# Kernel tuning notes

Hardware: AMD Instinct MI355X
Metric: run time of the kernel (lower is better)

## Reference

```python
import jax, jax.numpy as jnp
import numpy as np

LATENT, HIDDEN, NF, MAXN = 256, 512, 64, 50
B = 128
# ordered node pairs (i, j), i != j, in the original double-loop (row-major) order
_pairs = np.array([(i, j) for i in range(MAXN) for j in range(MAXN) if i != j], dtype=np.int32)
II = jnp.asarray(_pairs[:, 0])  # [P]
JJ = jnp.asarray(_pairs[:, 1])  # [P]


def _lin_init(key, out_d, in_d):
    kw, kb = jax.random.split(key)
    s = 1.0 / np.sqrt(in_d)
    W = jax.random.uniform(kw, (out_d, in_d), jnp.float32, -s, s)
    b = jax.random.uniform(kb, (out_d,), jnp.float32, -s, s)
    return W, b


def setup_inputs() -> dict:
    key = jax.random.key(0)
    ks = jax.random.split(key, 7)
    z = jax.random.normal(ks[0], (B, LATENT), jnp.float32)
    # node decoder: latent -> hidden -> hidden -> maxn*nf
    W1, b1 = _lin_init(ks[1], HIDDEN, LATENT)
    W2, b2 = _lin_init(ks[2], HIDDEN, HIDDEN)
    W3, b3 = _lin_init(ks[3], MAXN * NF, HIDDEN)
    # edge decoder: latent + 2*nf -> hidden -> hidden//2 -> 1
    E1, c1 = _lin_init(ks[4], HIDDEN, LATENT + 2 * NF)
    E2, c2 = _lin_init(ks[5], HIDDEN // 2, HIDDEN)
    E3, c3 = _lin_init(ks[6], 1, HIDDEN // 2)
    return {"z": z, "W1": W1, "b1": b1, "W2": W2, "b2": b2, "W3": W3, "b3": b3,
            "E1": E1, "c1": c1, "E2": E2, "c2": c2, "E3": E3, "c3": c3}


def reference(z, W1, b1, W2, b2, W3, b3, E1, c1, E2, c2, E3, c3):
    # ---- node decoder ----
    h = jax.nn.relu(z @ W1.T + b1)
    h = jax.nn.relu(h @ W2.T + b2)
    node_feat = (h @ W3.T + b3).reshape(B, MAXN, NF)  # raw logits used for edges
    node_probs = jax.nn.sigmoid(node_feat)
    # ---- edge decoder: batched over all P = MAXN*(MAXN-1) ordered pairs ----
    ni = node_feat[:, II, :]  # [B, P, NF]
    nj = node_feat[:, JJ, :]  # [B, P, NF]
    P = II.shape[0]
    zb = jnp.broadcast_to(z[:, None, :], (B, P, LATENT))
    edge_in = jnp.concatenate([zb, ni, nj], axis=-1)  # [B, P, LATENT+2*NF]
    e = jax.nn.relu(jnp.einsum("bpf,hf->bph", edge_in, E1) + c1)
    e = jax.nn.relu(jnp.einsum("bph,gh->bpg", e, E2) + c2)
    edge_probs = jax.nn.sigmoid(jnp.einsum("bpg,og->bpo", e, E3) + c3)[..., 0]  # [B, P]
    return node_probs, edge_probs
```

## Files before the change

kernel.cpp:

```cpp
#include <hip/hip_runtime.h>
#include <hip/hip_bf16.h>
#include <math.h>

#define LATENT 256
#define HIDDEN 512
#define NFD    64
#define MAXN   50
#define BATCH  128
#define NPAIR  2450
#define PTILE  64
#define NTILES 39

typedef __attribute__((ext_vector_type(8))) _Float16 f16x8;
typedef __attribute__((ext_vector_type(4))) float f32x4;
typedef __attribute__((ext_vector_type(4))) unsigned int u32x4;

__device__ __forceinline__ float sigmoidf_(float x) {
    return 1.0f / (1.0f + expf(-x));
}
__device__ __forceinline__ f16x8 build_e1(f16x8 ui, f16x8 uj) {
    f16x8 s = ui + uj;
    return __builtin_elementwise_max(s, (f16x8)(_Float16)0);
}
__device__ __forceinline__ u32x4 pack8(float4 a, float4 b) {
    f16x8 h;
    h[0] = (_Float16)a.x; h[1] = (_Float16)a.y;
    h[2] = (_Float16)a.z; h[3] = (_Float16)a.w;
    h[4] = (_Float16)b.x; h[5] = (_Float16)b.y;
    h[6] = (_Float16)b.z; h[7] = (_Float16)b.w;
    return __builtin_bit_cast(u32x4, h);
}

__global__ __launch_bounds__(256) void prologue_a(
    const float* __restrict__ z,
    const float* __restrict__ W1, const float* __restrict__ b1,
    const float* __restrict__ E1, const float* __restrict__ c1,
    const float* __restrict__ E2, const float* __restrict__ W2,
    const float* __restrict__ W3,
    unsigned short* __restrict__ E2t,
    unsigned short* __restrict__ W2t,
    unsigned short* __restrict__ W3t,
    unsigned short* __restrict__ E1ih,
    unsigned short* __restrict__ E1jh,
    unsigned short* __restrict__ h1h, float* __restrict__ Abc)
{
    const int tid = threadIdx.x;

    if (blockIdx.x >= 32) {
        int slot = (blockIdx.x - 32) * 4 + blockIdx.y;
        int e = (slot * 256 + tid) * 8;
        float4 a, b;
        unsigned short* dst;
        if (e < 262144) {
            int row = e >> 9, k = e & 511;
            a = *(const float4*)&W2[e];
            b = *(const float4*)&W2[e + 4];
            dst = W2t + (((k >> 3) * 512 + row) << 3);
        } else if (e < 1900544) {
            int l = e - 262144;
            int grow = l >> 9, k = l & 511;
            int node = grow >> 6, row = grow & 63;
            a = *(const float4*)&W3[l];
            b = *(const float4*)&W3[l + 4];
            dst = W3t + node * 32768 + (((k >> 3) * 64 + row) << 3);
        } else if (e < 1933312) {
            int l = e - 1900544; int row = l >> 6, col = l & 63;
            a = *(const float4*)&E1[row * 384 + 256 + col];
            b = *(const float4*)&E1[row * 384 + 260 + col];
            dst = E1ih + l;
        } else {
            int l = e - 1933312; int row = l >> 6, col = l & 63;
            a = *(const float4*)&E1[row * 384 + 320 + col];
            b = *(const float4*)&E1[row * 384 + 324 + col];
            dst = E1jh + l;
        }
        *(u32x4*)dst = pack8(a, b);
        return;
    }

    if (blockIdx.x >= 16) {
        int idx = ((blockIdx.x - 16) * 4 + blockIdx.y) * 256 + tid;
        int g  = idx & 255;
        int kc = idx >> 8;
        float4 a = *(const float4*)&E2[(size_t)g * 512 + kc * 8];
        float4 b = *(const float4*)&E2[(size_t)g * 512 + kc * 8 + 4];
        *(u32x4*)(E2t + (size_t)idx * 8) = pack8(a, b);
        return;
    }

    __shared__ __align__(16) float As[16][34];
    __shared__ __align__(16) float Bs[16][68];

    const int m0 = blockIdx.y * 32;
    const int n0 = blockIdx.x * 64;
    const bool isE = n0 >= 512;
    const float* Bp = isE ? E1 + (size_t)(n0 - 512) * 384 : W1 + (size_t)n0 * 256;
    const int ldb = isE ? 384 : 256;

    const int sra = tid >> 3;
    const int kca = (tid & 7) * 2;
    const int srb = tid >> 2;
    const int kcb = (tid & 3) * 4;
    const int tx = tid & 15;
    const int ty = tid >> 4;

    float acc[2][4] = {};

    for (int k0 = 0; k0 < 256; k0 += 16) {
        float2 a2 = *(const float2*)&z[(size_t)(m0 + sra) * 256 + k0 + kca];
        As[kca][sra] = a2.x; As[kca + 1][sra] = a2.y;
        float4 b4 = *(const float4*)&Bp[(size_t)srb * ldb + k0 + kcb];
        Bs[kcb + 0][srb] = b4.x; Bs[kcb + 1][srb] = b4.y;
        Bs[kcb + 2][srb] = b4.z; Bs[kcb + 3][srb] = b4.w;
        __syncthreads();
        #pragma unroll
        for (int k = 0; k < 16; ++k) {
            float av[2], bv[4];
            av[0] = As[k][ty * 2]; av[1] = As[k][ty * 2 + 1];
            *(float4*)bv = *(const float4*)&Bs[k][tx * 4];
            #pragma unroll
            for (int r = 0; r < 2; ++r)
                #pragma unroll
                for (int c = 0; c < 4; ++c)
                    acc[r][c] = fmaf(av[r], bv[c], acc[r][c]);
        }
        __syncthreads();
    }

    #pragma unroll
    for (int r = 0; r < 2; ++r) {
        int gm = m0 + ty * 2 + r;
        #pragma unroll
        for (int c = 0; c < 4; ++c) {
            int gn = n0 + tx * 4 + c;
            if (isE) {
                int gl = gn - 512;
                Abc[(size_t)gm * 512 + gl] = acc[r][c] + c1[gl];
            } else {
                float v = fmaxf(acc[r][c] + b1[gn], 0.f);
                h1h[(size_t)gm * 512 + gn] =
                    __builtin_bit_cast(unsigned short, (_Float16)v);
            }
        }
    }
}

__global__ __launch_bounds__(512, 1) void nfu_gemm(
    const unsigned short* __restrict__ h1h,
    const unsigned short* __restrict__ W2t,
    const float* __restrict__ b2,
    const unsigned short* __restrict__ W3t,
    const float* __restrict__ b3,
    const unsigned short* __restrict__ E1ih,
    const unsigned short* __restrict__ E1jh,
    const float* __restrict__ Abc,
    float* __restrict__ outN,
    unsigned short* __restrict__ Uih,
    unsigned short* __restrict__ Ujh)
{
    __shared__ unsigned short As[2][64 * 32];
    __shared__ __align__(16) unsigned short h2s[64][520];
    __shared__ __align__(16) unsigned short nft[64][72];

    const int tid = threadIdx.x;
    const int lane = tid & 63;
    const int w8 = tid >> 6;
    const int w  = w8 & 3;
    const int ln = lane & 15;
    const int hi = lane >> 4;
    const int node = blockIdx.x;
    const int m0 = blockIdx.y * 64;

    const int srow = (tid & 255) >> 2;
    const int sc   = tid & 3;
    const unsigned short* gA = h1h + (size_t)(m0 + srow) * 512 + sc * 8;
    const int swr = srow * 32 + ((sc ^ ((srow >> 1) & 3)) * 8);
    const int q   = hi ^ ((ln >> 1) & 3);
    const int ard = ln * 32 + q * 8;
    const unsigned short* bB = W2t + ((size_t)hi * 512 + 64 * w8 + ln) * 8;

    f32x4 acc[4][4] = {};
    f16x8 hN = {};
    if (tid < 256) {
        f16x8 h0 = *(const f16x8*)gA;
        *(f16x8*)&As[0][swr] = h0;
        hN = *(const f16x8*)(gA + 32);
    }
    f16x8 bf[4];
    #pragma unroll
    for (int ni = 0; ni < 4; ++ni)
        bf[ni] = *(const f16x8*)(bB + ni * 128);
    asm volatile("s_waitcnt lgkmcnt(0)\n\ts_barrier" ::: "memory");

    #pragma unroll
    for (int ks = 0; ks < 16; ++ks) {
        if (tid < 256 && ks < 15)
            *(f16x8*)&As[(ks + 1) & 1][swr] = hN;
        if (tid < 256 && ks < 14)
            hN = *(const f16x8*)(gA + 32 * (ks + 2));
        f16x8 af[4];
        #pragma unroll
        for (int mi = 0; mi < 4; ++mi)
            af[mi] = *(const f16x8*)&As[ks & 1][ard + mi * 512];
        __builtin_amdgcn_s_setprio(1);
        #pragma unroll
        for (int ni = 0; ni < 4; ++ni)
            #pragma unroll
            for (int mi = 0; mi < 4; ++mi)
                acc[mi][ni] = __builtin_amdgcn_mfma_f32_16x16x32_f16(
                    af[mi], bf[ni], acc[mi][ni], 0, 0, 0);
        __builtin_amdgcn_s_setprio(0);
        if (ks < 15) {
            #pragma unroll
            for (int ni = 0; ni < 4; ++ni)
                bf[ni] = *(const f16x8*)(bB + (size_t)(ks + 1) * 16384 + ni * 128);
            asm volatile("s_waitcnt lgkmcnt(0)\n\ts_barrier" ::: "memory");
        }
    }

    #pragma unroll
    for (int ni = 0; ni < 4; ++ni) {
        int col = 64 * w8 + 16 * ni + ln;
        float bias = b2[col];
        #pragma unroll
        for (int mi = 0; mi < 4; ++mi)
            #pragma unroll
            for (int r = 0; r < 4; ++r) {
                float v = fmaxf(acc[mi][ni][r] + bias, 0.f);
                h2s[16 * mi + 4 * hi + r][col] =
                    __builtin_bit_cast(unsigned short, (_Float16)v);
            }
    }
    __syncthreads();

    if (w8 < 4) {
        const unsigned short* bW3 = W3t + (size_t)node * 32768 + hi * 512 + ln * 8;
        f32x4 accB[4] = {};
        #pragma unroll
        for (int ks = 0; ks < 16; ++ks) {
            f16x8 af = *(const f16x8*)&h2s[16 * w + ln][ks * 32 + hi * 8];
            f16x8 bfB[4];
            #pragma unroll
            for (int ni = 0; ni < 4; ++ni)
                bfB[ni] = *(const f16x8*)(bW3 + ks * 2048 + ni * 128);
            #pragma unroll
            for (int ni = 0; ni < 4; ++ni)
                accB[ni] = __builtin_amdgcn_mfma_f32_16x16x32_f16(
                    af, bfB[ni], accB[ni], 0, 0, 0);
        }
        #pragma unroll
        for (int ni = 0; ni < 4; ++ni) {
            int gnl = 16 * ni + ln;
            int gng = node * 64 + gnl;
            float bias = b3[gng];
            #pragma unroll
            for (int r = 0; r < 4; ++r) {
                int bl = 16 * w + 4 * hi + r;
                float v = accB[ni][r] + bias;
                outN[(size_t)(m0 + bl) * 3200 + gng] = sigmoidf_(v);
                nft[bl][gnl] = __builtin_bit_cast(unsigned short, (_Float16)v);
            }
        }
    }
    __syncthreads();

    if (w8 < 4) {
        f16x8 af2[2][4];
        #pragma unroll
        for (int ks2 = 0; ks2 < 2; ++ks2)
            #pragma unroll
            for (int mi = 0; mi < 4; ++mi)
                af2[ks2][mi] = *(const f16x8*)&nft[16 * mi + ln][ks2 * 32 + hi * 8];

        #pragma unroll
        for (int ij = 0; ij < 2; ++ij) {
            const unsigned short* Ep = ij ? E1jh : E1ih;
            unsigned short* Ud = ij ? Ujh : Uih;
            #pragma unroll
            for (int half = 0; half < 2; ++half) {
                f32x4 acc2[4][4] = {};
                #pragma unroll
                for (int ks2 = 0; ks2 < 2; ++ks2) {
                    f16x8 bf2[4];
                    #pragma unroll
                    for (int ni = 0; ni < 4; ++ni)
                        bf2[ni] = *(const f16x8*)(Ep +
                            (size_t)(128 * w + half * 64 + 16 * ni + ln) * 64 +
                            ks2 * 32 + hi * 8);
                    #pragma unroll
                    for (int ni = 0; ni < 4; ++ni)
                        #pragma unroll
                        for (int mi = 0; mi < 4; ++mi)
                            acc2[mi][ni] = __builtin_amdgcn_mfma_f32_16x16x32_f16(
                                af2[ks2][mi], bf2[ni], acc2[mi][ni], 0, 0, 0);
                }
                #pragma unroll
                for (int mi = 0; mi < 4; ++mi) {
                    #pragma unroll
                    for (int r = 0; r < 4; ++r) {
                        int batch = m0 + 16 * mi + 4 * hi + r;
                        #pragma unroll
                        for (int ni = 0; ni < 4; ++ni) {
                            int h = 128 * w + half * 64 + 16 * ni + ln;
                            float v = acc2[mi][ni][r];
                            if (ij == 0) v += Abc[(size_t)batch * 512 + h];
                            Ud[((size_t)batch * 50 + node) * 512 + h] =
                                __builtin_bit_cast(unsigned short, (_Float16)v);
                        }
                    }
                }
            }
        }
    }
}

__global__ __launch_bounds__(256, 4) void edge_mfma(
    const unsigned short* __restrict__ Ui,
    const unsigned short* __restrict__ Uj,
    const unsigned short* __restrict__ E2t,
    const float* __restrict__ c2,
    const float* __restrict__ E3,
    const float* __restrict__ c3p,
    float* __restrict__ outE)
{
    __shared__ unsigned short As[2][PTILE * 32];
    __shared__ float c2_s[256], e3_s[256];
    __shared__ int   ii_s[PTILE], jj_s[PTILE];
    __shared__ float red[PTILE][5];

    const int gid = blockIdx.x;
    const int nid = (gid & 7) * 624 + (gid >> 3);
    const int b   = nid / NTILES;
    const int p0  = (nid - b * NTILES) * PTILE;

    const int tid = threadIdx.x;
    const int lane = tid & 63;
    const int wid  = tid >> 6;
    const int ln = lane & 15;
    const int hi = lane >> 4;

    c2_s[tid] = c2[tid];
    e3_s[tid] = E3[tid];
    if (tid < PTILE) {
        int p = p0 + tid;
        int i = 0, j = 0;
        if (p < NPAIR) {
            i = p / 49;
            int kk = p - i * 49;
            j = kk + (kk >= i ? 1 : 0);
        }
        ii_s[tid] = i;
        jj_s[tid] = j;
    }
    __syncthreads();

    const unsigned short* UiB = Ui + (size_t)b * MAXN * HIDDEN;
    const unsigned short* UjB = Uj + (size_t)b * MAXN * HIDDEN;

    const int srow = tid >> 2;
    const int sc   = tid & 3;
    const unsigned short* gUi = UiB + (size_t)ii_s[srow] * HIDDEN + sc * 8;
    const unsigned short* gUj = UjB + (size_t)jj_s[srow] * HIDDEN + sc * 8;
    const int swr = srow * 32 + ((sc ^ ((srow >> 1) & 3)) * 8);

    const int q   = hi ^ ((ln >> 1) & 3);
    const int ard = ln * 32 + q * 8;

    const unsigned short* bB = E2t + ((size_t)hi * 256 + 64 * wid + ln) * 8;

    f32x4 acc[4][4] = {};

    {
        f16x8 u0 = *(const f16x8*)gUi;
        f16x8 v0 = *(const f16x8*)gUj;
        *(f16x8*)&As[0][swr] = build_e1(u0, v0);
    }
    f16x8 uiN = *(const f16x8*)(gUi + 32);
    f16x8 ujN = *(const f16x8*)(gUj + 32);
    f16x8 bf[4];
    #pragma unroll
    for (int ni = 0; ni < 4; ++ni)
        bf[ni] = *(const f16x8*)(bB + ni * 128);
    asm volatile("s_waitcnt lgkmcnt(0)\n\ts_barrier" ::: "memory");

    #pragma unroll
    for (int ks = 0; ks < 16; ++ks) {
        if (ks < 15)
            *(f16x8*)&As[(ks + 1) & 1][swr] = build_e1(uiN, ujN);
        if (ks < 14) {
            uiN = *(const f16x8*)(gUi + 32 * (ks + 2));
            ujN = *(const f16x8*)(gUj + 32 * (ks + 2));
        }
        f16x8 af[4];
        #pragma unroll
        for (int mi = 0; mi < 4; ++mi)
            af[mi] = *(const f16x8*)&As[ks & 1][ard + mi * 512];
        __builtin_amdgcn_s_setprio(1);
        #pragma unroll
        for (int ni = 0; ni < 4; ++ni)
            #pragma unroll
            for (int mi = 0; mi < 4; ++mi)
                acc[mi][ni] = __builtin_amdgcn_mfma_f32_16x16x32_f16(
                    af[mi], bf[ni], acc[mi][ni], 0, 0, 0);
        __builtin_amdgcn_s_setprio(0);
        if (ks < 15) {
            #pragma unroll
            for (int ni = 0; ni < 4; ++ni)
                bf[ni] = *(const f16x8*)(bB + (size_t)(ks + 1) * 8192 + ni * 128);
            asm volatile("s_waitcnt lgkmcnt(0)\n\ts_barrier" ::: "memory");
        }
    }

    const float c3v = c3p[0];
    #pragma unroll
    for (int mi = 0; mi < 4; ++mi) {
        #pragma unroll
        for (int r = 0; r < 4; ++r) {
            float part = 0.f;
            #pragma unroll
            for (int ni = 0; ni < 4; ++ni) {
                int g = 64 * wid + 16 * ni + ln;
                float v = fmaxf(acc[mi][ni][r] + c2_s[g], 0.f);
                part = fmaf(v, e3_s[g], part);
            }
            part += __shfl_xor(part, 1);
            part += __shfl_xor(part, 2);
            part += __shfl_xor(part, 4);
            part += __shfl_xor(part, 8);
            if (ln == 0) red[16 * mi + 4 * hi + r][wid] = part;
        }
    }
    __syncthreads();

    if (tid < PTILE) {
        int p = p0 + tid;
        if (p < NPAIR) {
            float s = red[tid][0] + red[tid][1] + red[tid][2] + red[tid][3] + c3v;
            outE[(size_t)b * NPAIR + p] = sigmoidf_(s);
        }
    }
}

extern "C" void kernel_launch(void* const* d_in, const int* in_sizes, int n_in,
                              void* d_out, int out_size, void* d_ws, size_t ws_size,
                              hipStream_t stream)
{
    const float* z  = (const float*)d_in[0];
    const float* W1 = (const float*)d_in[1];
    const float* b1 = (const float*)d_in[2];
    const float* W2 = (const float*)d_in[3];
    const float* b2 = (const float*)d_in[4];
    const float* W3 = (const float*)d_in[5];
    const float* b3 = (const float*)d_in[6];
    const float* E1 = (const float*)d_in[7];
    const float* c1 = (const float*)d_in[8];
    const float* E2 = (const float*)d_in[9];
    const float* c2 = (const float*)d_in[10];
    const float* E3 = (const float*)d_in[11];
    const float* c3 = (const float*)d_in[12];

    float* out = (float*)d_out;
    float* ws  = (float*)d_ws;

    float* Abc = ws;
    unsigned short* h1h  = (unsigned short*)(Abc + 65536);
    unsigned short* W2t  = h1h + 65536;
    unsigned short* W3t  = W2t + 262144;
    unsigned short* E1ih = W3t + 1638400;
    unsigned short* E1jh = E1ih + 32768;
    unsigned short* E2t  = E1jh + 32768;
    unsigned short* Uih  = E2t + 131072;
    unsigned short* Ujh  = Uih + 3276800;

    dim3 blk(256);

    prologue_a<<<dim3(272, 4), blk, 0, stream>>>(
        z, W1, b1, E1, c1, E2, W2, W3, E2t, W2t, W3t, E1ih, E1jh, h1h, Abc);

    nfu_gemm<<<dim3(50, 2), dim3(512), 0, stream>>>(
        h1h, W2t, b2, W3t, b3, E1ih, E1jh, Abc, out, Uih, Ujh);

    edge_mfma<<<dim3(NTILES * BATCH), blk, 0, stream>>>(
        Uih, Ujh, E2t, c2, E3, c3, out + BATCH * MAXN * NFD);
}
```

Baseline: 124.7 us.

## Double K-step per LDS stage in edge MFMA loop with padded tile

The edge kernel's K loop now stages 64 columns of the fused Ui+Uj activation per LDS buffer instead of 32. That halves the number of barrier-synchronised iterations and issues two MFMA groups per stage. The LDS tile uses a padded row stride of 72 instead of an XOR swizzle to avoid bank conflicts, and the B fragments are double-buffered in registers. The occupancy hint drops from 4 to 3 blocks per SIMD to allow the extra registers, at the cost of fewer resident waves to hide latency.

```diff
diff --git a/kernel.cpp b/kernel.cpp
--- a/kernel.cpp
+++ b/kernel.cpp
@@ -314,7 +314,7 @@
     }
 }
 
-__global__ __launch_bounds__(256, 4) void edge_mfma(
+__global__ __launch_bounds__(256, 3) void edge_mfma(
     const unsigned short* __restrict__ Ui,
     const unsigned short* __restrict__ Uj,
     const unsigned short* __restrict__ E2t,
@@ -323,7 +323,7 @@
     const float* __restrict__ c3p,
     float* __restrict__ outE)
 {
-    __shared__ unsigned short As[2][PTILE * 32];
+    __shared__ unsigned short As[2][64 * 72];
     __shared__ float c2_s[256], e3_s[256];
     __shared__ int   ii_s[PTILE], jj_s[PTILE];
     __shared__ float red[PTILE][5];
@@ -361,52 +361,75 @@
     const int sc   = tid & 3;
     const unsigned short* gUi = UiB + (size_t)ii_s[srow] * HIDDEN + sc * 8;
     const unsigned short* gUj = UjB + (size_t)jj_s[srow] * HIDDEN + sc * 8;
-    const int swr = srow * 32 + ((sc ^ ((srow >> 1) & 3)) * 8);
-
-    const int q   = hi ^ ((ln >> 1) & 3);
-    const int ard = ln * 32 + q * 8;
+    const int swr0 = srow * 72 + sc * 8;
+    const int swr1 = srow * 72 + (sc + 4) * 8;
+
+    const int ard = ln * 72 + hi * 8;
 
     const unsigned short* bB = E2t + ((size_t)hi * 256 + 64 * wid + ln) * 8;
 
     f32x4 acc[4][4] = {};
 
     {
-        f16x8 u0 = *(const f16x8*)gUi;
-        f16x8 v0 = *(const f16x8*)gUj;
-        *(f16x8*)&As[0][swr] = build_e1(u0, v0);
-    }
-    f16x8 uiN = *(const f16x8*)(gUi + 32);
-    f16x8 ujN = *(const f16x8*)(gUj + 32);
-    f16x8 bf[4];
+        f16x8 a0 = *(const f16x8*)gUi;
+        f16x8 a1 = *(const f16x8*)(gUi + 32);
+        f16x8 b0 = *(const f16x8*)gUj;
+        f16x8 b1 = *(const f16x8*)(gUj + 32);
+        *(f16x8*)&As[0][swr0] = build_e1(a0, b0);
+        *(f16x8*)&As[0][swr1] = build_e1(a1, b1);
+    }
+    f16x8 uiN0 = *(const f16x8*)(gUi + 64);
+    f16x8 uiN1 = *(const f16x8*)(gUi + 96);
+    f16x8 ujN0 = *(const f16x8*)(gUj + 64);
+    f16x8 ujN1 = *(const f16x8*)(gUj + 96);
+    f16x8 bf0[4], bf1[4];
     #pragma unroll
     for (int ni = 0; ni < 4; ++ni)
-        bf[ni] = *(const f16x8*)(bB + ni * 128);
+        bf0[ni] = *(const f16x8*)(bB + ni * 128);
     asm volatile("s_waitcnt lgkmcnt(0)\n\ts_barrier" ::: "memory");
 
     #pragma unroll
-    for (int ks = 0; ks < 16; ++ks) {
-        if (ks < 15)
-            *(f16x8*)&As[(ks + 1) & 1][swr] = build_e1(uiN, ujN);
-        if (ks < 14) {
-            uiN = *(const f16x8*)(gUi + 32 * (ks + 2));
-            ujN = *(const f16x8*)(gUj + 32 * (ks + 2));
+    for (int w = 0; w < 8; ++w) {
+        #pragma unroll
+        for (int ni = 0; ni < 4; ++ni)
+            bf1[ni] = *(const f16x8*)(bB + (size_t)(2 * w + 1) * 8192 + ni * 128);
+        if (w < 7) {
+            *(f16x8*)&As[(w + 1) & 1][swr0] = build_e1(uiN0, ujN0);
+            *(f16x8*)&As[(w + 1) & 1][swr1] = build_e1(uiN1, ujN1);
+        }
+        if (w < 6) {
+            uiN0 = *(const f16x8*)(gUi + 64 * (w + 2));
+            uiN1 = *(const f16x8*)(gUi + 64 * (w + 2) + 32);
+            ujN0 = *(const f16x8*)(gUj + 64 * (w + 2));
+            ujN1 = *(const f16x8*)(gUj + 64 * (w + 2) + 32);
         }
         f16x8 af[4];
         #pragma unroll
         for (int mi = 0; mi < 4; ++mi)
-            af[mi] = *(const f16x8*)&As[ks & 1][ard + mi * 512];
+            af[mi] = *(const f16x8*)&As[w & 1][ard + mi * 1152];
         __builtin_amdgcn_s_setprio(1);
         #pragma unroll
         for (int ni = 0; ni < 4; ++ni)
             #pragma unroll
             for (int mi = 0; mi < 4; ++mi)
                 acc[mi][ni] = __builtin_amdgcn_mfma_f32_16x16x32_f16(
-                    af[mi], bf[ni], acc[mi][ni], 0, 0, 0);
+                    af[mi], bf0[ni], acc[mi][ni], 0, 0, 0);
         __builtin_amdgcn_s_setprio(0);
-        if (ks < 15) {
+        #pragma unroll
+        for (int mi = 0; mi < 4; ++mi)
+            af[mi] = *(const f16x8*)&As[w & 1][ard + 32 + mi * 1152];
+        __builtin_amdgcn_s_setprio(1);
+        #pragma unroll
+        for (int ni = 0; ni < 4; ++ni)
+            #pragma unroll
+            for (int mi = 0; mi < 4; ++mi)
+                acc[mi][ni] = __builtin_amdgcn_mfma_f32_16x16x32_f16(
+                    af[mi], bf1[ni], acc[mi][ni], 0, 0, 0);
+        __builtin_amdgcn_s_setprio(0);
+        if (w < 7) {
             #pragma unroll
             for (int ni = 0; ni < 4; ++ni)
-                bf[ni] = *(const f16x8*)(bB + (size_t)(ks + 1) * 8192 + ni * 128);
+                bf0[ni] = *(const f16x8*)(bB + (size_t)(2 * w + 2) * 8192 + ni * 128);
             asm volatile("s_waitcnt lgkmcnt(0)\n\ts_barrier" ::: "memory");
         }
     }
```

Result: slower. 127.8 us (+2.5%).
